# Kernel tuning notes

Hardware: AMD Instinct MI355X
Metric: run time of the kernel (lower is better)

Reference implementation:

```python
import jax, jax.numpy as jnp
import numpy as np
import math

VOCAB, D, L, H, DFF, S, B = 32000, 1024, 6, 16, 4096, 512, 4
DK = D // H
EPS = 1e-6


def layernorm(x, g, b):
    # Faithful to source: divides by (std + eps), std is population std (unbiased=False)
    mu = jnp.mean(x, axis=-1, keepdims=True)
    std = jnp.sqrt(jnp.mean((x - mu) ** 2, axis=-1, keepdims=True))
    return g * (x - mu) / (std + EPS) + b


def setup_inputs() -> dict:
    key = jax.random.key(0)
    ks = jax.random.split(key, 12)
    s = 0.02
    inp = {
        "tokens": jax.random.randint(ks[0], (B, S), 0, VOCAB, dtype=jnp.int32),
        "tok_emb": jax.random.normal(ks[1], (VOCAB, D), jnp.float32) * s,
        "pos_emb": jax.random.normal(ks[2], (1, S, D), jnp.float32) * s,
        # per-layer stacked params [L, ...]
        "Wq": jax.random.normal(ks[3], (L, D, D), jnp.float32) * s,
        "bq": jnp.zeros((L, D), jnp.float32),
        "Wk": jax.random.normal(ks[4], (L, D, D), jnp.float32) * s,
        "bk": jnp.zeros((L, D), jnp.float32),
        "Wv": jax.random.normal(ks[5], (L, D, D), jnp.float32) * s,
        "bv": jnp.zeros((L, D), jnp.float32),
        "Wo": jax.random.normal(ks[6], (L, D, D), jnp.float32) * s,
        "bo": jnp.zeros((L, D), jnp.float32),
        "g1": jnp.ones((L, D), jnp.float32),
        "be1": jnp.zeros((L, D), jnp.float32),
        "W1": jax.random.normal(ks[7], (L, D, DFF), jnp.float32) * s,
        "bf1": jnp.zeros((L, DFF), jnp.float32),
        "W2": jax.random.normal(ks[8], (L, DFF, D), jnp.float32) * s,
        "bf2": jnp.zeros((L, D), jnp.float32),
        "g2": jnp.ones((L, D), jnp.float32),
        "be2": jnp.zeros((L, D), jnp.float32),
        "gf": jnp.ones((D,), jnp.float32),
        "bf": jnp.zeros((D,), jnp.float32),
    }
    return inp


def gpt_forward(tokens, tok_emb, pos_emb, Wq, bq, Wk, bk, Wv, bv, Wo, bo,
                g1, be1, W1, bf1, W2, bf2, g2, be2, gf, bf):
    seq = tokens.shape[1]
    x = tok_emb[tokens] * math.sqrt(D) + pos_emb[:, :seq, :]  # [B,S,D]
    causal = jnp.tril(jnp.ones((seq, seq), bool))  # [S,S]

    def block(x, p):
        wq, bq_, wk, bk_, wv, bv_, wo, bo_, g1_, be1_, w1, bf1_, w2, bf2_, g2_, be2_ = p
        h = layernorm(x, g1_, be1_)
        q = (h @ wq + bq_).reshape(B, seq, H, DK).transpose(0, 2, 1, 3)  # [B,H,S,DK]
        k = (h @ wk + bk_).reshape(B, seq, H, DK).transpose(0, 2, 1, 3)
        v = (h @ wv + bv_).reshape(B, seq, H, DK).transpose(0, 2, 1, 3)
        scores = jnp.einsum("bhqd,bhkd->bhqk", q, k) / math.sqrt(DK)
        scores = jnp.where(causal, scores, -1e9)
        p_attn = jax.nn.softmax(scores, axis=-1)
        attn = jnp.einsum("bhqk,bhkd->bhqd", p_attn, v)
        attn = attn.transpose(0, 2, 1, 3).reshape(B, seq, D)
        x = x + (attn @ wo + bo_)
        h2 = layernorm(x, g2_, be2_)
        ff = jnp.maximum(h2 @ w1 + bf1_, 0.0) @ w2 + bf2_
        return x + ff, None

    params = (Wq, bq, Wk, bk, Wv, bv, Wo, bo, g1, be1, W1, bf1, W2, bf2, g2, be2)
    x, _ = jax.lax.scan(block, x, params)
    x = layernorm(x, gf, bf)
    logits = x @ tok_emb.T  # tied head, no bias
    return logits


def reference(tokens, tok_emb, pos_emb, Wq, bq, Wk, bk, Wv, bv, Wo, bo,
              g1, be1, W1, bf1, W2, bf2, g2, be2, gf, bf):
    return gpt_forward(tokens, tok_emb, pos_emb, Wq, bq, Wk, bk, Wv, bv, Wo, bo,
                       g1, be1, W1, bf1, W2, bf2, g2, be2, gf, bf)
```

## Files before the change

### kernel.cpp

```cpp
#include <hip/hip_runtime.h>

#define TOKENS 2048
#define DM 1024
#define NHEAD 16
#define DH 64
#define SEQL 512
#define NBATCH 4
#define DFFN 4096
#define NLAYER 6
#define NVOCAB 32000

typedef short short8 __attribute__((ext_vector_type(8)));
typedef short short4v __attribute__((ext_vector_type(4)));
typedef float floatx4 __attribute__((ext_vector_type(4)));

#define FLAG_RELU 1
#define FLAG_OUTBF16 2

#define AS1 __attribute__((address_space(1)))
#define AS3 __attribute__((address_space(3)))

__device__ __forceinline__ float bf2f(short s) {
  unsigned u = ((unsigned)(unsigned short)s) << 16;
  return __builtin_bit_cast(float, u);
}
__device__ __forceinline__ short f2bf(float f) {
  unsigned u = __builtin_bit_cast(unsigned, f);
  u = (u + 0x7FFFu + ((u >> 16) & 1u)) >> 16;
  return (short)(unsigned short)u;
}

template<int N> __device__ __forceinline__ void wait_vm() {
  if constexpr (N == 0)      asm volatile("s_waitcnt vmcnt(0)" ::: "memory");
  else if constexpr (N == 3) asm volatile("s_waitcnt vmcnt(3)" ::: "memory");
  else if constexpr (N == 4) asm volatile("s_waitcnt vmcnt(4)" ::: "memory");
  else if constexpr (N == 6) asm volatile("s_waitcnt vmcnt(6)" ::: "memory");
  else if constexpr (N == 8) asm volatile("s_waitcnt vmcnt(8)" ::: "memory");
  else static_assert(N == 0, "unsupported vmcnt");
}

template<int BM, int BN, int WR, int WC, int BK>
__global__ __launch_bounds__(256) void gemm_db(
    const short* __restrict__ A, const short* __restrict__ Bt, void* __restrict__ Cv,
    const float* __restrict__ bias, const float* __restrict__ resid,
    int K, int lda, int ldb, int ldc, float alpha, int flags)
{
  constexpr int FI = BM / WR / 16;
  constexpr int FJ = BN / WC / 16;
  constexpr int RPI = (BK == 64) ? 32 : 64;
  constexpr int NST = BM / RPI + BN / RPI;
  __shared__ short As[2][BM * BK];
  __shared__ short Bs[2][BN * BK];

  const int gy = gridDim.y;
  int lin = blockIdx.x + gridDim.x * blockIdx.y;
  const int nwg = gridDim.x * gy;
  if ((nwg & 7) == 0) { const int cpx = nwg >> 3; lin = (lin & 7) * cpx + (lin >> 3); }
  const int row0 = (lin % gy) * BM, col0 = (lin / gy) * BN;

  const int tid = threadIdx.x;
  const int lane = tid & 63;
  const int wid = tid >> 6;
  const int wr = wid / WC, wc = wid % WC;
  const int lc = lane & 15, g = lane >> 4;
  const int sr = (BK == 64) ? (tid >> 3) : (tid >> 2);
  const int sc = (BK == 64) ? (tid & 7) : (tid & 3);
  const int swz_s = (BK == 64) ? (sr & 7) : ((sr >> 1) & 3);
  const int scs = (sc ^ swz_s) * 8;

  floatx4 acc[FI][FJ];
  #pragma unroll
  for (int i = 0; i < FI; ++i)
    #pragma unroll
    for (int j = 0; j < FJ; ++j)
      acc[i][j] = (floatx4){0.f, 0.f, 0.f, 0.f};

  auto stage = [&](int k0, int b) {
    char* ad = (char*)As[b];
    char* bd = (char*)Bs[b];
    #pragma unroll
    for (int it = 0; it < BM / RPI; ++it) {
      const short* src = A + (long)(row0 + it * RPI + sr) * lda + k0 + scs;
      __builtin_amdgcn_global_load_lds((const AS1 void*)src,
          (AS3 void*)(ad + it * 4096 + tid * 16), 16, 0, 0);
    }
    #pragma unroll
    for (int it = 0; it < BN / RPI; ++it) {
      const short* src = Bt + (long)(col0 + it * RPI + sr) * ldb + k0 + scs;
      __builtin_amdgcn_global_load_lds((const AS1 void*)src,
          (AS3 void*)(bd + it * 4096 + tid * 16), 16, 0, 0);
    }
  };

  const int NT = K / BK;
  stage(0, 0);
  int cb = 0;
  for (int t = 0; t < NT; ++t) {
    __builtin_amdgcn_s_barrier();
    __builtin_amdgcn_sched_barrier(0);
    if (t + 1 < NT) {
      stage((t + 1) * BK, cb ^ 1);
      wait_vm<NST>();
    } else {
      wait_vm<0>();
    }
    __builtin_amdgcn_sched_barrier(0);

    const short* as = As[cb];
    const short* bs = Bs[cb];
    if constexpr (BK == 64) {
      short8 fa[FI][2], fb[FJ][2];
      #pragma unroll
      for (int i = 0; i < FI; ++i) {
        const int r = wr * (BM / WR) + i * 16 + lc;
        fa[i][0] = *(const short8*)&as[r * 64 + ((g ^ (r & 7)) * 8)];
        fa[i][1] = *(const short8*)&as[r * 64 + (((4 + g) ^ (r & 7)) * 8)];
      }
      #pragma unroll
      for (int j = 0; j < FJ; ++j) {
        const int r = wc * (BN / WC) + j * 16 + lc;
        fb[j][0] = *(const short8*)&bs[r * 64 + ((g ^ (r & 7)) * 8)];
        fb[j][1] = *(const short8*)&bs[r * 64 + (((4 + g) ^ (r & 7)) * 8)];
      }
      #pragma unroll
      for (int i = 0; i < FI; ++i)
        #pragma unroll
        for (int j = 0; j < FJ; ++j) {
          acc[i][j] = __builtin_amdgcn_mfma_f32_16x16x32_bf16(fa[i][0], fb[j][0], acc[i][j], 0, 0, 0);
          acc[i][j] = __builtin_amdgcn_mfma_f32_16x16x32_bf16(fa[i][1], fb[j][1], acc[i][j], 0, 0, 0);
        }
    } else {
      short8 fa[FI], fb[FJ];
      #pragma unroll
      for (int i = 0; i < FI; ++i) {
        const int r = wr * (BM / WR) + i * 16 + lc;
        fa[i] = *(const short8*)&as[r * 32 + ((g ^ ((r >> 1) & 3)) * 8)];
      }
      #pragma unroll
      for (int j = 0; j < FJ; ++j) {
        const int r = wc * (BN / WC) + j * 16 + lc;
        fb[j] = *(const short8*)&bs[r * 32 + ((g ^ ((r >> 1) & 3)) * 8)];
      }
      #pragma unroll
      for (int i = 0; i < FI; ++i)
        #pragma unroll
        for (int j = 0; j < FJ; ++j)
          acc[i][j] = __builtin_amdgcn_mfma_f32_16x16x32_bf16(fa[i], fb[j], acc[i][j], 0, 0, 0);
    }
    cb ^= 1;
  }

  const bool relu = flags & FLAG_RELU;
  const bool obf  = flags & FLAG_OUTBF16;
  float* Cf = (float*)Cv;
  short* Cb = (short*)Cv;
  #pragma unroll
  for (int i = 0; i < FI; ++i) {
    int orow = row0 + wr * (BM / WR) + i * 16 + g * 4;
    #pragma unroll
    for (int j = 0; j < FJ; ++j) {
      int ocol = col0 + wc * (BN / WC) + j * 16 + lc;
      #pragma unroll
      for (int t = 0; t < 4; ++t) {
        long off = (long)(orow + t) * ldc + ocol;
        float v = alpha * acc[i][j][t];
        if (bias)  v += bias[ocol];
        if (resid) v += resid[off];
        if (relu)  v = fmaxf(v, 0.f);
        if (obf) Cb[off] = f2bf(v); else Cf[off] = v;
      }
    }
  }
}

template<int BM, int BN, int WR, int WC, int BK>
static inline void launch_gemm(hipStream_t st, const short* A, const short* Bt, void* C,
    const float* bias, const float* resid, int M, int N, int K,
    int lda, int ldb, int ldc, float alpha, int flags)
{
  dim3 grid(N / BN, M / BM, 1), blk(256);
  gemm_db<BM, BN, WR, WC, BK><<<grid, blk, 0, st>>>(A, Bt, C, bias, resid,
                                                    K, lda, ldb, ldc, alpha, flags);
}

__global__ __launch_bounds__(256) void flash_attn(
    const short* __restrict__ qkv, const short* __restrict__ Vt,
    short* __restrict__ attn)
{
  const int qt = blockIdx.x;
  const int bh = blockIdx.y;
  const int b = bh >> 4, h = bh & 15;
  const int row0 = qt * 64;

  __shared__ short Kt[64 * 64];
  __shared__ short Vtl[64 * 64];
  __shared__ short Pt[4 * 16 * 64];

  const int tid = threadIdx.x;
  const int lane = tid & 63;
  const int wid = tid >> 6;
  const int lc = lane & 15, g = lane >> 4;

  short8 qf[2];
  {
    const short* qp = qkv + (long)(b * SEQL + row0 + wid * 16 + lc) * 3072 + h * DH;
    qf[0] = *(const short8*)(qp + g * 8);
    qf[1] = *(const short8*)(qp + 32 + g * 8);
  }

  floatx4 o[4];
  float m[4], l[4];
  #pragma unroll
  for (int j = 0; j < 4; ++j) o[j] = (floatx4){0.f, 0.f, 0.f, 0.f};
  #pragma unroll
  for (int t = 0; t < 4; ++t) { m[t] = -3e38f; l[t] = 0.f; }

  for (int kv0 = 0; kv0 <= row0; kv0 += 64) {
    #pragma unroll
    for (int i = 0; i < 2; ++i) {
      const int idx = i * 256 + tid;
      const int r = idx >> 3, cc = idx & 7;
      const int sw = cc ^ (r & 7);
      const short* ks = qkv + (long)(b * SEQL + kv0 + r) * 3072 + 1024 + h * DH + sw * 8;
      __builtin_amdgcn_global_load_lds((const AS1 void*)ks,
          (AS3 void*)((char*)Kt + (i * 256 + wid * 64) * 16), 16, 0, 0);
      const short* vs = Vt + (long)bh * DH * SEQL + (long)r * SEQL + kv0 + sw * 8;
      __builtin_amdgcn_global_load_lds((const AS1 void*)vs,
          (AS3 void*)((char*)Vtl + (i * 256 + wid * 64) * 16), 16, 0, 0);
    }
    __syncthreads();

    floatx4 s[4];
    #pragma unroll
    for (int j = 0; j < 4; ++j) s[j] = (floatx4){0.f, 0.f, 0.f, 0.f};
    #pragma unroll
    for (int ks_ = 0; ks_ < 2; ++ks_) {
      #pragma unroll
      for (int j = 0; j < 4; ++j) {
        const int row = j * 16 + lc;
        const short8 kf = *(const short8*)&Kt[row * 64 + ((ks_ * 4 + g) ^ (row & 7)) * 8];
        s[j] = __builtin_amdgcn_mfma_f32_16x16x32_bf16(qf[ks_], kf, s[j], 0, 0, 0);
      }
    }

    const bool diag = (kv0 == row0);
    float p[4][4], rmax[4], rsum[4], fs[4];
    #pragma unroll
    for (int t = 0; t < 4; ++t) rmax[t] = -3e38f;
    #pragma unroll
    for (int j = 0; j < 4; ++j)
      #pragma unroll
      for (int t = 0; t < 4; ++t) {
        float sv = s[j][t] * 0.125f;
        if (diag && (j * 16 + lc) > (wid * 16 + g * 4 + t)) sv = -3e38f;
        p[j][t] = sv;
        rmax[t] = fmaxf(rmax[t], sv);
      }
    #pragma unroll
    for (int t = 0; t < 4; ++t) {
      #pragma unroll
      for (int mk = 1; mk < 16; mk <<= 1)
        rmax[t] = fmaxf(rmax[t], __shfl_xor(rmax[t], mk));
      float mn = fmaxf(m[t], rmax[t]);
      fs[t] = __expf(m[t] - mn);
      m[t] = mn;
    }
    #pragma unroll
    for (int j = 0; j < 4; ++j)
      #pragma unroll
      for (int t = 0; t < 4; ++t)
        p[j][t] = __expf(p[j][t] - m[t]);
    #pragma unroll
    for (int t = 0; t < 4; ++t) {
      rsum[t] = p[0][t] + p[1][t] + p[2][t] + p[3][t];
      #pragma unroll
      for (int mk = 1; mk < 16; mk <<= 1)
        rsum[t] += __shfl_xor(rsum[t], mk);
      l[t] = l[t] * fs[t] + rsum[t];
    }
    #pragma unroll
    for (int j = 0; j < 4; ++j) {
      o[j][0] *= fs[0]; o[j][1] *= fs[1]; o[j][2] *= fs[2]; o[j][3] *= fs[3];
    }
    #pragma unroll
    for (int j = 0; j < 4; ++j)
      #pragma unroll
      for (int t = 0; t < 4; ++t) {
        const int r = g * 4 + t;
        const int col = j * 16 + lc;
        Pt[wid * 1024 + r * 64 + (((col >> 3) ^ (r & 7)) * 8) + (col & 7)] = f2bf(p[j][t]);
      }
    __syncthreads();

    #pragma unroll
    for (int ks_ = 0; ks_ < 2; ++ks_) {
      const short8 pf = *(const short8*)&Pt[wid * 1024 + lc * 64 + ((ks_ * 4 + g) ^ (lc & 7)) * 8];
      #pragma unroll
      for (int j = 0; j < 4; ++j) {
        const int row = j * 16 + lc;
        const short8 vf = *(const short8*)&Vtl[row * 64 + ((ks_ * 4 + g) ^ (row & 7)) * 8];
        o[j] = __builtin_amdgcn_mfma_f32_16x16x32_bf16(pf, vf, o[j], 0, 0, 0);
      }
    }
    __syncthreads();
  }

  float linv[4];
  #pragma unroll
  for (int t = 0; t < 4; ++t) linv[t] = 1.f / l[t];
  #pragma unroll
  for (int j = 0; j < 4; ++j)
    #pragma unroll
    for (int t = 0; t < 4; ++t) {
      const long row = (long)(b * SEQL + row0 + wid * 16 + g * 4 + t);
      attn[row * DM + h * DH + j * 16 + lc] = f2bf(o[j][t] * linv[t]);
    }
}

__global__ __launch_bounds__(256) void ln_bf16(const float* __restrict__ x,
    const float* __restrict__ gg, const float* __restrict__ bb, short* __restrict__ out)
{
  int row = blockIdx.x;
  const float4 u = ((const float4*)(x + (long)row * DM))[threadIdx.x];
  float s  = u.x + u.y + u.z + u.w;
  float sq = u.x * u.x + u.y * u.y + u.z * u.z + u.w * u.w;
  #pragma unroll
  for (int o = 32; o; o >>= 1) { s += __shfl_xor(s, o); sq += __shfl_xor(sq, o); }
  __shared__ float red[8];
  int lane = threadIdx.x & 63, wid = threadIdx.x >> 6;
  if (lane == 0) { red[wid] = s; red[4 + wid] = sq; }
  __syncthreads();
  s  = red[0] + red[1] + red[2] + red[3];
  sq = red[4] + red[5] + red[6] + red[7];
  float mu  = s * (1.f / DM);
  float var = fmaxf(sq * (1.f / DM) - mu * mu, 0.f);
  float inv = 1.f / (sqrtf(var) + 1e-6f);
  int c = threadIdx.x * 4;
  const float4 gv = ((const float4*)gg)[threadIdx.x];
  const float4 bv = ((const float4*)bb)[threadIdx.x];
  short4v o;
  o[0] = f2bf((u.x - mu) * inv * gv.x + bv.x);
  o[1] = f2bf((u.y - mu) * inv * gv.y + bv.y);
  o[2] = f2bf((u.z - mu) * inv * gv.z + bv.z);
  o[3] = f2bf((u.w - mu) * inv * gv.w + bv.w);
  *(short4v*)(out + (long)row * DM + c) = o;
}

__global__ __launch_bounds__(256) void embed_k(const int* __restrict__ toks,
    const float* __restrict__ emb, const float* __restrict__ pos, float* __restrict__ x)
{
  int row = blockIdx.x;
  int s = row & (SEQL - 1);
  long tk = toks[row];
  const float4 e = ((const float4*)(emb + tk * DM))[threadIdx.x];
  const float4 p = ((const float4*)(pos + (long)s * DM))[threadIdx.x];
  float4 o;
  o.x = e.x * 32.f + p.x; o.y = e.y * 32.f + p.y;
  o.z = e.z * 32.f + p.z; o.w = e.w * 32.f + p.w;
  ((float4*)(x + (long)row * DM))[threadIdx.x] = o;
}

__global__ void wtrans(const float* __restrict__ W, short* __restrict__ Wt,
                       int K, int N, long zsout)
{
  __shared__ float tile[32][33];
  const long lo = (long)blockIdx.z * K * N;
  const long oo = (long)blockIdx.z * zsout;
  int n0 = blockIdx.x * 32, k0 = blockIdx.y * 32;
  int tx = threadIdx.x, ty = threadIdx.y;
  #pragma unroll
  for (int i = 0; i < 4; ++i)
    tile[ty + i * 8][tx] = W[lo + (long)(k0 + ty + i * 8) * N + n0 + tx];
  __syncthreads();
  #pragma unroll
  for (int i = 0; i < 4; ++i)
    Wt[oo + (long)(n0 + ty + i * 8) * K + k0 + tx] = f2bf(tile[tx][ty + i * 8]);
}

__global__ __launch_bounds__(256) void conv_bf16(const float* __restrict__ in,
                                                 short* __restrict__ out)
{
  long i = ((long)blockIdx.x * 256 + threadIdx.x) * 8;
  float4 a = *(const float4*)(in + i);
  float4 b = *(const float4*)(in + i + 4);
  short8 o;
  o[0] = f2bf(a.x); o[1] = f2bf(a.y); o[2] = f2bf(a.z); o[3] = f2bf(a.w);
  o[4] = f2bf(b.x); o[5] = f2bf(b.y); o[6] = f2bf(b.z); o[7] = f2bf(b.w);
  *(short8*)(out + i) = o;
}

__global__ void vtrans(const short* __restrict__ qkv, short* __restrict__ Vt)
{
  __shared__ short tile[32][33];
  int bh = blockIdx.z;
  int b = bh >> 4, h = bh & 15;
  int s0 = blockIdx.x * 32, d0 = blockIdx.y * 32;
  int tx = threadIdx.x, ty = threadIdx.y;
  #pragma unroll
  for (int i = 0; i < 4; ++i)
    tile[ty + i * 8][tx] =
        qkv[((long)(b * SEQL + s0 + ty + i * 8)) * 3072 + 2048 + h * DH + d0 + tx];
  __syncthreads();
  #pragma unroll
  for (int i = 0; i < 4; ++i)
    Vt[((long)(bh * DH + d0 + ty + i * 8)) * SEQL + s0 + tx] = tile[tx][ty + i * 8];
}

__global__ void bias_cat(const float* __restrict__ bq, const float* __restrict__ bk,
                         const float* __restrict__ bv, float* __restrict__ out)
{
  int l = blockIdx.y;
  int i = blockIdx.x * 256 + threadIdx.x;
  float v = (i < 1024) ? bq[l * 1024 + i]
          : (i < 2048) ? bk[l * 1024 + i - 1024]
                       : bv[l * 1024 + i - 2048];
  out[(long)l * 3072 + i] = v;
}

extern "C" void kernel_launch(void* const* d_in, const int* in_sizes, int n_in,
                              void* d_out, int out_size, void* d_ws, size_t ws_size,
                              hipStream_t stream)
{
  (void)in_sizes; (void)n_in; (void)out_size;
  const int*   toks = (const int*)  d_in[0];
  const float* temb = (const float*)d_in[1];
  const float* pemb = (const float*)d_in[2];
  const float* Wq  = (const float*)d_in[3];  const float* bq  = (const float*)d_in[4];
  const float* Wk  = (const float*)d_in[5];  const float* bk  = (const float*)d_in[6];
  const float* Wv  = (const float*)d_in[7];  const float* bv  = (const float*)d_in[8];
  const float* Wo  = (const float*)d_in[9];  const float* bo  = (const float*)d_in[10];
  const float* g1  = (const float*)d_in[11]; const float* be1 = (const float*)d_in[12];
  const float* W1  = (const float*)d_in[13]; const float* bf1 = (const float*)d_in[14];
  const float* W2  = (const float*)d_in[15]; const float* bf2 = (const float*)d_in[16];
  const float* g2  = (const float*)d_in[17]; const float* be2 = (const float*)d_in[18];
  const float* gf  = (const float*)d_in[19]; const float* bfb = (const float*)d_in[20];

  char* p = (char*)d_ws;
  auto carve = [&](size_t bytes) -> char* {
    char* r = p;
    p += (bytes + 255) & ~(size_t)255;
    return r;
  };
  short* h     = (short*)carve((size_t)TOKENS * DM * 2);
  char*  uni   = p;
  short* tembb = (short*)uni;
  short* Wqkvt = (short*)carve((size_t)NLAYER * 3072 * DM * 2);
  short* Wot   = (short*)carve((size_t)NLAYER * DM * DM * 2);
  short* W1t   = (short*)carve((size_t)NLAYER * DM * DFFN * 2);
  short* W2t   = (short*)carve((size_t)NLAYER * DM * DFFN * 2);
  float* x     = (float*)carve((size_t)TOKENS * DM * 4);
  short* qkv   = (short*)carve((size_t)TOKENS * 3072 * 2);
  short* attn  = (short*)carve((size_t)TOKENS * DM * 2);
  short* Vt    = (short*)carve((size_t)NBATCH * NHEAD * DH * SEQL * 2);
  short* ffb   = (short*)carve((size_t)TOKENS * DFFN * 2);
  float* bqkv  = (float*)carve((size_t)NLAYER * 3072 * 4);
  size_t used = (size_t)(p - (char*)d_ws);
  size_t need_t = (size_t)(uni - (char*)d_ws) + (size_t)NVOCAB * DM * 2;
  if (used > ws_size || need_t > ws_size) return;

  dim3 tb(32, 8);

  embed_k<<<TOKENS, 256, 0, stream>>>(toks, temb, pemb, x);
  bias_cat<<<dim3(12, NLAYER), 256, 0, stream>>>(bq, bk, bv, bqkv);
  wtrans<<<dim3(DM / 32, DM / 32, NLAYER), tb, 0, stream>>>(Wq, Wqkvt, DM, DM, 3072L * DM);
  wtrans<<<dim3(DM / 32, DM / 32, NLAYER), tb, 0, stream>>>(Wk, Wqkvt + (size_t)DM * DM, DM, DM, 3072L * DM);
  wtrans<<<dim3(DM / 32, DM / 32, NLAYER), tb, 0, stream>>>(Wv, Wqkvt + (size_t)2 * DM * DM, DM, DM, 3072L * DM);
  wtrans<<<dim3(DM / 32, DM / 32, NLAYER), tb, 0, stream>>>(Wo, Wot, DM, DM, (long)DM * DM);
  wtrans<<<dim3(DFFN / 32, DM / 32, NLAYER), tb, 0, stream>>>(W1, W1t, DM, DFFN, (long)DM * DFFN);
  wtrans<<<dim3(DM / 32, DFFN / 32, NLAYER), tb, 0, stream>>>(W2, W2t, DFFN, DM, (long)DM * DFFN);

  for (int l = 0; l < NLAYER; ++l) {
    const size_t wqkv = (size_t)l * 3072 * DM;
    const size_t wdd  = (size_t)l * DM * DM;
    const size_t wdf  = (size_t)l * DM * DFFN;
    ln_bf16<<<TOKENS, 256, 0, stream>>>(x, g1 + l * DM, be1 + l * DM, h);
    launch_gemm<128, 128, 2, 2, 64>(stream, h, Wqkvt + wqkv, qkv, bqkv + (size_t)l * 3072,
        nullptr, TOKENS, 3072, DM, DM, DM, 3072, 1.f, FLAG_OUTBF16);
    vtrans<<<dim3(SEQL / 32, DH / 32, NBATCH * NHEAD), tb, 0, stream>>>(qkv, Vt);
    flash_attn<<<dim3(SEQL / 64, NBATCH * NHEAD), 256, 0, stream>>>(qkv, Vt, attn);
    launch_gemm<64, 128, 1, 4, 64>(stream, attn, Wot + wdd, x, bo + l * DM, x,
        TOKENS, DM, DM, DM, DM, DM, 1.f, 0);
    ln_bf16<<<TOKENS, 256, 0, stream>>>(x, g2 + l * DM, be2 + l * DM, h);
    launch_gemm<128, 128, 2, 2, 64>(stream, h, W1t + wdf, ffb, bf1 + l * DFFN, nullptr,
        TOKENS, DFFN, DM, DM, DM, DFFN, 1.f, FLAG_OUTBF16 | FLAG_RELU);
    launch_gemm<64, 128, 1, 4, 64>(stream, ffb, W2t + wdf, x, bf2 + l * DM, x,
        TOKENS, DM, DFFN, DFFN, DFFN, DM, 1.f, 0);
  }
  ln_bf16<<<TOKENS, 256, 0, stream>>>(x, gf, bfb, h);
  conv_bf16<<<(NVOCAB * DM) / (256 * 8), 256, 0, stream>>>(temb, tembb);
  launch_gemm<128, 128, 2, 2, 32>(stream, h, tembb, d_out, nullptr, nullptr,
      TOKENS, NVOCAB, DM, DM, DM, NVOCAB, 1.f, 0);
}
```

Baseline: 1.548 ms.

## Add 256x256-tile GEMM with 8 waves for the vocab logits head

Introduces a dedicated GEMM kernel for the tied-embedding output projection using 256x256 block tiles, 512 threads, direct global-to-LDS loads with XOR-swizzled layout, double buffering, and an XCD-aware workgroup remap. Larger tiles raise arithmetic intensity and cut the number of workgroups for the largest GEMM (2048x32000x1024). The remap spreads consecutive tiles across chiplets to improve L2 locality. In exchange it uses much more LDS and registers per block, which lowers occupancy, and output stores are uncoalesced scalar fp32 writes.

```diff
diff --git a/kernel.cpp b/kernel.cpp
--- a/kernel.cpp
+++ b/kernel.cpp
@@ -181,6 +181,100 @@
   dim3 grid(N / BN, M / BM, 1), blk(256);
   gemm_db<BM, BN, WR, WC, BK><<<grid, blk, 0, st>>>(A, Bt, C, bias, resid,
                                                     K, lda, ldb, ldc, alpha, flags);
+}
+
+__global__ __launch_bounds__(512, 2) void gemm256h(
+    const short* __restrict__ A, const short* __restrict__ Bt, float* __restrict__ C,
+    int K, int lda, int ldb, int ldc)
+{
+  __shared__ short As[2][256 * 32];
+  __shared__ short Bs[2][256 * 32];
+
+  const int gy = gridDim.y;
+  int lin = blockIdx.x + gridDim.x * blockIdx.y;
+  const int nwg = gridDim.x * gy;
+  if ((nwg & 7) == 0) { const int cpx = nwg >> 3; lin = (lin & 7) * cpx + (lin >> 3); }
+  const int row0 = (lin % gy) * 256, col0 = (lin / gy) * 256;
+
+  const int tid = threadIdx.x;
+  const int lane = tid & 63;
+  const int w = tid >> 6;
+  const int wr = w >> 2, wc = w & 3;
+  const int lc = lane & 15, g = lane >> 4;
+  const int sr = tid >> 2;
+  const int sc = tid & 3;
+  const int scs = (sc ^ ((sr >> 1) & 3)) * 8;
+
+  floatx4 acc[8][4];
+  #pragma unroll
+  for (int i = 0; i < 8; ++i)
+    #pragma unroll
+    for (int j = 0; j < 4; ++j)
+      acc[i][j] = (floatx4){0.f, 0.f, 0.f, 0.f};
+
+  auto stage = [&](int k0, int b) {
+    char* ad = (char*)As[b];
+    char* bd = (char*)Bs[b];
+    #pragma unroll
+    for (int it = 0; it < 2; ++it) {
+      const short* src = A + (long)(row0 + it * 128 + sr) * lda + k0 + scs;
+      __builtin_amdgcn_global_load_lds((const AS1 void*)src,
+          (AS3 void*)(ad + it * 8192 + tid * 16), 16, 0, 0);
+    }
+    #pragma unroll
+    for (int it = 0; it < 2; ++it) {
+      const short* src = Bt + (long)(col0 + it * 128 + sr) * ldb + k0 + scs;
+      __builtin_amdgcn_global_load_lds((const AS1 void*)src,
+          (AS3 void*)(bd + it * 8192 + tid * 16), 16, 0, 0);
+    }
+  };
+
+  const int NT = K >> 5;
+  stage(0, 0);
+  int cb = 0;
+  for (int t = 0; t < NT; ++t) {
+    __builtin_amdgcn_s_barrier();
+    __builtin_amdgcn_sched_barrier(0);
+    if (t + 1 < NT) {
+      stage((t + 1) << 5, cb ^ 1);
+      wait_vm<4>();
+    } else {
+      wait_vm<0>();
+    }
+    __builtin_amdgcn_sched_barrier(0);
+
+    const short* as = As[cb];
+    const short* bs = Bs[cb];
+    short8 fa[8], fb[4];
+    #pragma unroll
+    for (int i = 0; i < 8; ++i) {
+      const int r = wr * 128 + i * 16 + lc;
+      fa[i] = *(const short8*)&as[r * 32 + ((g ^ ((r >> 1) & 3)) * 8)];
+    }
+    #pragma unroll
+    for (int j = 0; j < 4; ++j) {
+      const int r = wc * 64 + j * 16 + lc;
+      fb[j] = *(const short8*)&bs[r * 32 + ((g ^ ((r >> 1) & 3)) * 8)];
+    }
+    #pragma unroll
+    for (int i = 0; i < 8; ++i)
+      #pragma unroll
+      for (int j = 0; j < 4; ++j)
+        acc[i][j] = __builtin_amdgcn_mfma_f32_16x16x32_bf16(fa[i], fb[j], acc[i][j], 0, 0, 0);
+    cb ^= 1;
+  }
+
+  #pragma unroll
+  for (int i = 0; i < 8; ++i) {
+    int orow = row0 + wr * 128 + i * 16 + g * 4;
+    #pragma unroll
+    for (int j = 0; j < 4; ++j) {
+      int ocol = col0 + wc * 64 + j * 16 + lc;
+      #pragma unroll
+      for (int t = 0; t < 4; ++t)
+        C[(long)(orow + t) * ldc + ocol] = acc[i][j][t];
+    }
+  }
 }
 
 __global__ __launch_bounds__(256) void flash_attn(
@@ -488,6 +582,8 @@
   }
   ln_bf16<<<TOKENS, 256, 0, stream>>>(x, gf, bfb, h);
   conv_bf16<<<(NVOCAB * DM) / (256 * 8), 256, 0, stream>>>(temb, tembb);
-  launch_gemm<128, 128, 2, 2, 32>(stream, h, tembb, d_out, nullptr, nullptr,
-      TOKENS, NVOCAB, DM, DM, DM, NVOCAB, 1.f, 0);
-}
+  {
+    dim3 grid(NVOCAB / 256, TOKENS / 256, 1), blk(512);
+    gemm256h<<<grid, blk, 0, stream>>>(h, tembb, (float*)d_out, DM, DM, DM, NVOCAB);
+  }
+}
```

Result: no change. 1.557 ms (+0.5%).
